# Optimization experiments

Hardware: AMD Instinct MI355X
Metric: run time of the kernel (lower is better)

## Reference

```python
import jax, jax.numpy as jnp
import numpy as np

NUM_C = 100000
EMB = 256
NUM_LEVEL = 8
PRETRAIN = 768
B, L = 64, 200


def setup_inputs() -> dict:
    key = jax.random.key(0)
    k1, k2, k3, k4, k5, k6, k7 = jax.random.split(key, 7)
    croutes = jax.random.randint(k1, (B, L, NUM_LEVEL), -2, NUM_C)  # -2 == padding
    tailcs = jax.random.randint(k2, (B, L), 0, NUM_C)
    cid_emb = jax.random.normal(k3, (NUM_C, EMB), dtype=jnp.float32)
    weight = jax.random.normal(k4, (NUM_LEVEL,), dtype=jnp.float32)
    # RobertaEncode: frozen pretrained table [num_c+2, pretrain_dim] + Linear(pretrain_dim, emb_size)
    content_table = jax.random.normal(k5, (NUM_C + 2, PRETRAIN), dtype=jnp.float32) * 0.02
    proj_w = jax.random.normal(k6, (PRETRAIN, EMB), dtype=jnp.float32) * (PRETRAIN ** -0.5)
    proj_b = jax.random.normal(k7, (EMB,), dtype=jnp.float32) * 0.01
    return {"croutes": croutes, "tailcs": tailcs, "cid_emb": cid_emb,
            "weight": weight, "content_table": content_table,
            "proj_w": proj_w, "proj_b": proj_b}


def reference(croutes, tailcs, cid_emb, weight, content_table, proj_w, proj_b):
    # emb_type = 'qid_rcadd', model_name = 'akt_peiyou' -> route-encoding branch
    emb_size = cid_emb.shape[1]
    # cat 2 zero rows (for padding -2 and -1) in front of cid_emb
    concept_emb_cat = jnp.concatenate(
        [jnp.zeros((2, emb_size), cid_emb.dtype), cid_emb], axis=0)  # [num_c+2, E]
    related = (croutes + 2).astype(jnp.int32)                        # [B,L,K]
    cemb1 = concept_emb_cat[related]                                 # [B,L,K,E]
    # content_emb(croutes+2): gather pretrained rows, linear projection (dropout=eval identity)
    cemb2 = content_table[related] @ proj_w + proj_b                 # [B,L,K,E]
    cemb = cemb1 + cemb2                                             # 'rcadd'
    # masked softmax over levels: weight[level] where available else -inf
    is_avail = related != 0                                          # [B,L,K]
    new_weights = jnp.where(is_avail, weight, -jnp.inf)              # broadcast weight[K]
    alphas = jax.nn.softmax(new_weights, axis=-1)                    # [B,L,K]
    out = jnp.einsum('blk,blke->ble', alphas, cemb)                  # weighted pool
    return out
```

## Files before the change

kernel.cpp:

```cpp
#include <hip/hip_runtime.h>
#include <hip/hip_bf16.h>

#define EMB 256
#define PRETRAIN 768
#define NLEV 8
#define BLK 12800

typedef __attribute__((ext_vector_type(8))) short short8t;
typedef __attribute__((ext_vector_type(4))) float f32x4;

static __device__ __forceinline__ unsigned short f2b(float f) {
    unsigned u = __builtin_bit_cast(unsigned, f);
    u += 0x7fffu + ((u >> 16) & 1u);
    return (unsigned short)(u >> 16);
}

__global__ __launch_bounds__(256) void pool_kernel(
    const int* __restrict__ croutes,
    const float* __restrict__ cid_emb,
    const float* __restrict__ weight,
    const float* __restrict__ content,
    const float* __restrict__ proj_w,
    unsigned short* __restrict__ pooled,
    unsigned short* __restrict__ WT,
    float* __restrict__ out)
{
    const int t = threadIdx.x;

    if (blockIdx.x >= BLK) {
        const int g  = (blockIdx.x - BLK) * 256 + t;
        const int n  = g & 255;
        const int kb = (g >> 8) << 3;
        short8t v;
#pragma unroll
        for (int j = 0; j < 8; ++j)
            v[j] = (short)f2b(proj_w[(size_t)(kb + j) * EMB + n]);
        *(short8t*)(WT + (size_t)n * PRETRAIN + kb) = v;
        return;
    }

    const int bl = blockIdx.x;

    int   idx[NLEV];
    float alpha[NLEV];
    float m = -INFINITY;
#pragma unroll
    for (int k = 0; k < NLEV; ++k) {
        idx[k] = croutes[bl * NLEV + k] + 2;
        if (idx[k] != 0) m = fmaxf(m, weight[k]);
    }
    float s = 0.f;
#pragma unroll
    for (int k = 0; k < NLEV; ++k) {
        float e = (idx[k] != 0) ? expf(weight[k] - m) : 0.f;
        alpha[k] = e;
        s += e;
    }
    const float inv = 1.f / s;
#pragma unroll
    for (int k = 0; k < NLEV; ++k) alpha[k] *= inv;

    if (t < 192) {
        float ax = 0.f, ay = 0.f, az = 0.f, aw = 0.f;
#pragma unroll
        for (int k = 0; k < NLEV; ++k) {
            if (idx[k] != 0) {
                const float4* row = (const float4*)(content + (size_t)idx[k] * PRETRAIN);
                float4 v = row[t];
                float  a = alpha[k];
                ax = fmaf(a, v.x, ax); ay = fmaf(a, v.y, ay);
                az = fmaf(a, v.z, az); aw = fmaf(a, v.w, aw);
            }
        }
        ushort4 o;
        o.x = f2b(ax); o.y = f2b(ay); o.z = f2b(az); o.w = f2b(aw);
        *(ushort4*)(pooled + (size_t)bl * PRETRAIN + t * 4) = o;
    } else {
        const int tc = t - 192;
        float ax = 0.f, ay = 0.f, az = 0.f, aw = 0.f;
#pragma unroll
        for (int k = 0; k < NLEV; ++k) {
            if (idx[k] >= 2) {
                const float4* row = (const float4*)(cid_emb + (size_t)(idx[k] - 2) * EMB);
                float4 v = row[tc];
                float  a = alpha[k];
                ax = fmaf(a, v.x, ax); ay = fmaf(a, v.y, ay);
                az = fmaf(a, v.z, az); aw = fmaf(a, v.w, aw);
            }
        }
        float4 o = {ax, ay, az, aw};
        *(float4*)(out + (size_t)bl * EMB + tc * 4) = o;
    }
}

__global__ __launch_bounds__(256) void gemm_kernel(
    const unsigned short* __restrict__ A,
    const unsigned short* __restrict__ WT,
    const float* __restrict__ proj_b,
    float* __restrict__ out)
{
    __shared__ char smem[8192 + 16384];
    char* sA = smem;
    char* sB = smem + 8192;

    const int t    = threadIdx.x;
    const int lane = t & 63;
    const int wave = t >> 6;
    const int wr   = wave >> 1, wc = wave & 1;
    const int bm0  = blockIdx.x * 64;
    const int bn0  = blockIdx.y * 128;

    f32x4 acc[2][4] = {};

    for (int k0 = 0; k0 < PRETRAIN; k0 += 64) {
#pragma unroll
        for (int i = 0; i < 2; ++i) {
            int c = t + i * 256;
            int row = c >> 3, cc = c & 7;
            short8t v = *(const short8t*)(A + (size_t)(bm0 + row) * PRETRAIN + k0 + cc * 8);
            *(short8t*)(sA + row * 128 + ((cc * 16) ^ ((row & 7) << 4))) = v;
        }
#pragma unroll
        for (int i = 0; i < 4; ++i) {
            int c = t + i * 256;
            int row = c >> 3, cc = c & 7;
            short8t v = *(const short8t*)(WT + (size_t)(bn0 + row) * PRETRAIN + k0 + cc * 8);
            *(short8t*)(sB + row * 128 + ((cc * 16) ^ ((row & 7) << 4))) = v;
        }
        __syncthreads();
#pragma unroll
        for (int ks = 0; ks < 2; ++ks) {
            const int kb = ks * 64 + (lane >> 4) * 16;
            short8t a[2], b[4];
#pragma unroll
            for (int mf = 0; mf < 2; ++mf) {
                int row = wr * 32 + mf * 16 + (lane & 15);
                a[mf] = *(const short8t*)(sA + row * 128 + (kb ^ ((row & 7) << 4)));
            }
#pragma unroll
            for (int nf = 0; nf < 4; ++nf) {
                int n = wc * 64 + nf * 16 + (lane & 15);
                b[nf] = *(const short8t*)(sB + n * 128 + (kb ^ ((n & 7) << 4)));
            }
#pragma unroll
            for (int mf = 0; mf < 2; ++mf)
#pragma unroll
                for (int nf = 0; nf < 4; ++nf)
                    acc[mf][nf] = __builtin_amdgcn_mfma_f32_16x16x32_bf16(
                        a[mf], b[nf], acc[mf][nf], 0, 0, 0);
        }
        __syncthreads();
    }

#pragma unroll
    for (int mf = 0; mf < 2; ++mf)
#pragma unroll
        for (int nf = 0; nf < 4; ++nf)
#pragma unroll
            for (int i = 0; i < 4; ++i) {
                int mrow = bm0 + wr * 32 + mf * 16 + (lane >> 4) * 4 + i;
                int ncol = bn0 + wc * 64 + nf * 16 + (lane & 15);
                size_t o = (size_t)mrow * EMB + ncol;
                out[o] = out[o] + acc[mf][nf][i] + proj_b[ncol];
            }
}

extern "C" void kernel_launch(void* const* d_in, const int* in_sizes, int n_in,
                              void* d_out, int out_size, void* d_ws, size_t ws_size,
                              hipStream_t stream) {
    const int*   croutes = (const int*)d_in[0];
    const float* cid_emb = (const float*)d_in[2];
    const float* weight  = (const float*)d_in[3];
    const float* content = (const float*)d_in[4];
    const float* proj_w  = (const float*)d_in[5];
    const float* proj_b  = (const float*)d_in[6];
    float*       out     = (float*)d_out;

    char* ws = (char*)d_ws;
    unsigned short* pooled = (unsigned short*)ws;
    unsigned short* WT     = (unsigned short*)(ws + 19660800);

    pool_kernel<<<BLK + 96, 256, 0, stream>>>(croutes, cid_emb, weight, content,
                                              proj_w, pooled, WT, out);
    gemm_kernel<<<dim3(200, 2), 256, 0, stream>>>(pooled, WT, proj_b, out);
}
```

Measured before the change: 481.6 us.

## Batch gather loads in pool kernel and double-buffer GEMM with smaller N tiles

The pool kernel now issues all eight row loads unconditionally before the FMAs. Padded rows read row 0 of the content table or a clamped cid_emb row, with a zero weight, so the loads can all be in flight at once instead of being serialized behind branches. The GEMM switches to 64x64 tiles with an 800-block grid and a register-staged double-buffered shared memory pipeline that prefetches the next K slice during the MFMAs. This targets memory latency in both kernels, at the cost of some extra wasted loads for padding rows and more registers.

```diff
diff --git a/kernel.cpp b/kernel.cpp
--- a/kernel.cpp
+++ b/kernel.cpp
@@ -61,32 +61,37 @@
     for (int k = 0; k < NLEV; ++k) alpha[k] *= inv;
 
     if (t < 192) {
+        float4 v[NLEV];
+#pragma unroll
+        for (int k = 0; k < NLEV; ++k)
+            v[k] = ((const float4*)(content + (size_t)idx[k] * PRETRAIN))[t];
         float ax = 0.f, ay = 0.f, az = 0.f, aw = 0.f;
 #pragma unroll
         for (int k = 0; k < NLEV; ++k) {
-            if (idx[k] != 0) {
-                const float4* row = (const float4*)(content + (size_t)idx[k] * PRETRAIN);
-                float4 v = row[t];
-                float  a = alpha[k];
-                ax = fmaf(a, v.x, ax); ay = fmaf(a, v.y, ay);
-                az = fmaf(a, v.z, az); aw = fmaf(a, v.w, aw);
-            }
+            float a = alpha[k];
+            ax = fmaf(a, v[k].x, ax); ay = fmaf(a, v[k].y, ay);
+            az = fmaf(a, v[k].z, az); aw = fmaf(a, v[k].w, aw);
         }
         ushort4 o;
         o.x = f2b(ax); o.y = f2b(ay); o.z = f2b(az); o.w = f2b(aw);
         *(ushort4*)(pooled + (size_t)bl * PRETRAIN + t * 4) = o;
     } else {
         const int tc = t - 192;
+        float4 v[NLEV];
+        float  a2[NLEV];
+#pragma unroll
+        for (int k = 0; k < NLEV; ++k) {
+            int r   = idx[k] - 2;
+            a2[k]   = (r >= 0) ? alpha[k] : 0.f;
+            r       = (r < 0) ? 0 : r;
+            v[k] = ((const float4*)(cid_emb + (size_t)r * EMB))[tc];
+        }
         float ax = 0.f, ay = 0.f, az = 0.f, aw = 0.f;
 #pragma unroll
         for (int k = 0; k < NLEV; ++k) {
-            if (idx[k] >= 2) {
-                const float4* row = (const float4*)(cid_emb + (size_t)(idx[k] - 2) * EMB);
-                float4 v = row[tc];
-                float  a = alpha[k];
-                ax = fmaf(a, v.x, ax); ay = fmaf(a, v.y, ay);
-                az = fmaf(a, v.z, az); aw = fmaf(a, v.w, aw);
-            }
+            float a = a2[k];
+            ax = fmaf(a, v[k].x, ax); ay = fmaf(a, v[k].y, ay);
+            az = fmaf(a, v[k].z, az); aw = fmaf(a, v[k].w, aw);
         }
         float4 o = {ax, ay, az, aw};
         *(float4*)(out + (size_t)bl * EMB + tc * 4) = o;
@@ -99,67 +104,85 @@
     const float* __restrict__ proj_b,
     float* __restrict__ out)
 {
-    __shared__ char smem[8192 + 16384];
-    char* sA = smem;
-    char* sB = smem + 8192;
+    __shared__ char smem[32768];
 
     const int t    = threadIdx.x;
     const int lane = t & 63;
     const int wave = t >> 6;
     const int wr   = wave >> 1, wc = wave & 1;
     const int bm0  = blockIdx.x * 64;
-    const int bn0  = blockIdx.y * 128;
-
-    f32x4 acc[2][4] = {};
-
-    for (int k0 = 0; k0 < PRETRAIN; k0 += 64) {
-#pragma unroll
-        for (int i = 0; i < 2; ++i) {
-            int c = t + i * 256;
-            int row = c >> 3, cc = c & 7;
-            short8t v = *(const short8t*)(A + (size_t)(bm0 + row) * PRETRAIN + k0 + cc * 8);
-            *(short8t*)(sA + row * 128 + ((cc * 16) ^ ((row & 7) << 4))) = v;
-        }
-#pragma unroll
-        for (int i = 0; i < 4; ++i) {
-            int c = t + i * 256;
-            int row = c >> 3, cc = c & 7;
-            short8t v = *(const short8t*)(WT + (size_t)(bn0 + row) * PRETRAIN + k0 + cc * 8);
-            *(short8t*)(sB + row * 128 + ((cc * 16) ^ ((row & 7) << 4))) = v;
-        }
-        __syncthreads();
+    const int bn0  = blockIdx.y * 64;
+
+    const int c0 = t, c1 = t + 256;
+    const int r0 = c0 >> 3, cc0 = c0 & 7;
+    const int r1 = c1 >> 3, cc1 = c1 & 7;
+    const size_t aoff0 = (size_t)(bm0 + r0) * PRETRAIN + cc0 * 8;
+    const size_t aoff1 = (size_t)(bm0 + r1) * PRETRAIN + cc1 * 8;
+    const size_t boff0 = (size_t)(bn0 + r0) * PRETRAIN + cc0 * 8;
+    const size_t boff1 = (size_t)(bn0 + r1) * PRETRAIN + cc1 * 8;
+    const int wA0 = r0 * 128 + ((cc0 * 16) ^ ((r0 & 7) << 4));
+    const int wA1 = r1 * 128 + ((cc1 * 16) ^ ((r1 & 7) << 4));
+
+    f32x4 acc[2][2] = {};
+
+    short8t va0 = *(const short8t*)(A + aoff0);
+    short8t va1 = *(const short8t*)(A + aoff1);
+    short8t vb0 = *(const short8t*)(WT + boff0);
+    short8t vb1 = *(const short8t*)(WT + boff1);
+    *(short8t*)(smem + wA0)        = va0;
+    *(short8t*)(smem + wA1)        = va1;
+    *(short8t*)(smem + 8192 + wA0) = vb0;
+    *(short8t*)(smem + 8192 + wA1) = vb1;
+    __syncthreads();
+
+    for (int tt = 0; tt < 12; ++tt) {
+        char* cbuf = smem + (tt & 1) * 16384;
+        char* nbuf = smem + ((tt + 1) & 1) * 16384;
+        if (tt < 11) {
+            const int k0 = (tt + 1) * 64;
+            va0 = *(const short8t*)(A + aoff0 + k0);
+            va1 = *(const short8t*)(A + aoff1 + k0);
+            vb0 = *(const short8t*)(WT + boff0 + k0);
+            vb1 = *(const short8t*)(WT + boff1 + k0);
+        }
 #pragma unroll
         for (int ks = 0; ks < 2; ++ks) {
             const int kb = ks * 64 + (lane >> 4) * 16;
-            short8t a[2], b[4];
+            short8t a[2], b[2];
 #pragma unroll
             for (int mf = 0; mf < 2; ++mf) {
                 int row = wr * 32 + mf * 16 + (lane & 15);
-                a[mf] = *(const short8t*)(sA + row * 128 + (kb ^ ((row & 7) << 4)));
+                a[mf] = *(const short8t*)(cbuf + row * 128 + (kb ^ ((row & 7) << 4)));
             }
 #pragma unroll
-            for (int nf = 0; nf < 4; ++nf) {
-                int n = wc * 64 + nf * 16 + (lane & 15);
-                b[nf] = *(const short8t*)(sB + n * 128 + (kb ^ ((n & 7) << 4)));
+            for (int nf = 0; nf < 2; ++nf) {
+                int n = wc * 32 + nf * 16 + (lane & 15);
+                b[nf] = *(const short8t*)(cbuf + 8192 + n * 128 + (kb ^ ((n & 7) << 4)));
             }
 #pragma unroll
             for (int mf = 0; mf < 2; ++mf)
 #pragma unroll
-                for (int nf = 0; nf < 4; ++nf)
+                for (int nf = 0; nf < 2; ++nf)
                     acc[mf][nf] = __builtin_amdgcn_mfma_f32_16x16x32_bf16(
                         a[mf], b[nf], acc[mf][nf], 0, 0, 0);
         }
+        if (tt < 11) {
+            *(short8t*)(nbuf + wA0)        = va0;
+            *(short8t*)(nbuf + wA1)        = va1;
+            *(short8t*)(nbuf + 8192 + wA0) = vb0;
+            *(short8t*)(nbuf + 8192 + wA1) = vb1;
+        }
         __syncthreads();
     }
 
 #pragma unroll
     for (int mf = 0; mf < 2; ++mf)
 #pragma unroll
-        for (int nf = 0; nf < 4; ++nf)
+        for (int nf = 0; nf < 2; ++nf)
 #pragma unroll
             for (int i = 0; i < 4; ++i) {
                 int mrow = bm0 + wr * 32 + mf * 16 + (lane >> 4) * 4 + i;
-                int ncol = bn0 + wc * 64 + nf * 16 + (lane & 15);
+                int ncol = bn0 + wc * 32 + nf * 16 + (lane & 15);
                 size_t o = (size_t)mrow * EMB + ncol;
                 out[o] = out[o] + acc[mf][nf][i] + proj_b[ncol];
             }
@@ -182,5 +205,5 @@
 
     pool_kernel<<<BLK + 96, 256, 0, stream>>>(croutes, cid_emb, weight, content,
                                               proj_w, pooled, WT, out);
-    gemm_kernel<<<dim3(200, 2), 256, 0, stream>>>(pooled, WT, proj_b, out);
-}
+    gemm_kernel<<<dim3(200, 4), 256, 0, stream>>>(pooled, WT, proj_b, out);
+}
```

Result: no change. 476.6 us (-1.0%).
